# Kernel optimization log

Measured on AMD Instinct MI355X. Metric: run time of the kernel, lower is better.

The kernel has to match this reference:

```python
import jax, jax.numpy as jnp
import numpy as np

N = 100000   # nodes per node type
E = 1000000  # edges per edge type
C = 128      # channels
H = 4        # num_heads
D = C // H   # head_dim


def setup_inputs() -> dict:
    key = jax.random.key(0)
    ks = jax.random.split(key, 16)
    return {
        "x_A": jax.random.normal(ks[0], (N, C), jnp.float32),
        "x_B": jax.random.normal(ks[1], (N, C), jnp.float32),
        "Wq": jax.random.normal(ks[2], (C, C), jnp.float32) * 0.05,
        "bq": jax.random.normal(ks[3], (C,), jnp.float32) * 0.05,
        "Wk": jax.random.normal(ks[4], (C, C), jnp.float32) * 0.05,
        "bk": jax.random.normal(ks[5], (C,), jnp.float32) * 0.05,
        "Wv": jax.random.normal(ks[6], (C, C), jnp.float32) * 0.05,
        "bv": jax.random.normal(ks[7], (C,), jnp.float32) * 0.05,
        "gamma": jnp.ones((C,), jnp.float32),
        "beta": jnp.zeros((C,), jnp.float32),
        "bias_AB": jax.random.normal(ks[8], (1,), jnp.float32),
        "bias_BA": jax.random.normal(ks[9], (1,), jnp.float32),
        "sb_AB": jax.random.normal(ks[10], (E,), jnp.float32),
        "sb_BA": jax.random.normal(ks[11], (E,), jnp.float32),
        "edge_index_AB": jax.random.randint(ks[12], (2, E), 0, N, jnp.int32),
        "edge_index_BA": jax.random.randint(ks[13], (2, E), 0, N, jnp.int32),
    }


def _edge_attention(x_src, x_dst, src, dst, sb, etype_bias, Wq, bq, Wk, bk, Wv, bv):
    """Per-edge-type attention: gather -> score -> dst-segment softmax -> scatter-add."""
    n_dst = x_dst.shape[0]
    Q = (x_dst @ Wq.T + bq).reshape(n_dst, H, D)
    K = (x_src @ Wk.T + bk).reshape(-1, H, D)
    V = (x_src @ Wv.T + bv).reshape(-1, H, D)
    # [E, H] per-edge scores
    scores = jnp.einsum('ehd,ehd->eh', Q[dst], K[src]) / np.float32(np.sqrt(D))
    scores = scores + sb[:, None] + etype_bias  # spatial bias + edge-type bias
    # segment softmax over edges grouped by dst node (numerically stable)
    m = jax.ops.segment_max(scores, dst, num_segments=n_dst)
    ex = jnp.exp(scores - m[dst])
    denom = jax.ops.segment_sum(ex, dst, num_segments=n_dst)
    w = ex / denom[dst]  # [E, H]
    msg = (V[src] * w[:, :, None]).reshape(-1, C)  # [E, C]
    return jax.ops.segment_sum(msg, dst, num_segments=n_dst)  # index_add_


def _layernorm(x, gamma, beta, eps=1e-5):
    mu = x.mean(-1, keepdims=True)
    var = ((x - mu) ** 2).mean(-1, keepdims=True)
    return (x - mu) / jnp.sqrt(var + eps) * gamma + beta


def _forward(x_A, x_B, Wq, bq, Wk, bk, Wv, bv, gamma, beta,
             bias_AB, bias_BA, sb_AB, sb_BA, edge_index_AB, edge_index_BA):
    src_ab, dst_ab = edge_index_AB[0], edge_index_AB[1]  # A -> B
    src_ba, dst_ba = edge_index_BA[0], edge_index_BA[1]  # B -> A
    lin = (Wq, bq, Wk, bk, Wv, bv)
    out_B = _edge_attention(x_A, x_B, src_ab, dst_ab, sb_AB, bias_AB, *lin)
    out_A = _edge_attention(x_B, x_A, src_ba, dst_ba, sb_BA, bias_BA, *lin)
    # total degree = in_deg + out_deg per node type
    ones_e = jnp.ones((E,), jnp.float32)
    deg_A = (jax.ops.segment_sum(ones_e, src_ab, num_segments=N)
             + jax.ops.segment_sum(ones_e, dst_ba, num_segments=N))
    deg_B = (jax.ops.segment_sum(ones_e, dst_ab, num_segments=N)
             + jax.ops.segment_sum(ones_e, src_ba, num_segments=N))
    out_A = out_A + deg_A[:, None]
    out_B = out_B + deg_B[:, None]
    out_A = _layernorm(out_A + x_A, gamma, beta)
    out_B = _layernorm(out_B + x_B, gamma, beta)
    return out_A, out_B


def reference(x_A, x_B, Wq, bq, Wk, bk, Wv, bv, gamma, beta,
              bias_AB, bias_BA, sb_AB, sb_BA, edge_index_AB, edge_index_BA):
    return _forward(x_A, x_B, Wq, bq, Wk, bk, Wv, bv, gamma, beta,
                    bias_AB, bias_BA, sb_AB, sb_BA, edge_index_AB, edge_index_BA)
```

## Files before the change

### kernel.cpp

```cpp
#include <hip/hip_runtime.h>

#define CH 128
#define QSCALE (0.17677669529663687f * 1.4426950408889634f)
#define LOG2E 1.4426950408889634f
#define SCAN_BLK 1024
#define KVSTRIDE 384
#define QROWS 32
#define WCVT_BLOCKS 192

typedef _Float16 f16;
typedef _Float16 f16x2 __attribute__((ext_vector_type(2)));
typedef _Float16 f16x8 __attribute__((ext_vector_type(8)));
typedef __attribute__((ext_vector_type(4))) float f32x4;

__device__ __forceinline__ unsigned pk2(float a, float b) {
    auto h = __builtin_amdgcn_cvt_pkrtz(a, b);
    return __builtin_bit_cast(unsigned, h);
}
__device__ __forceinline__ f16x2 u2h(unsigned u) { return __builtin_bit_cast(f16x2, u); }

template <int CTRL>
__device__ __forceinline__ float dpp_add(float x) {
    const int t = __builtin_amdgcn_update_dpp(0, __builtin_bit_cast(int, x), CTRL, 0xF, 0xF, false);
    return x + __builtin_bit_cast(float, t);
}
__device__ __forceinline__ float head_sum(float x) {
    x = dpp_add<0xB1>(x);
    x = dpp_add<0x4E>(x);
    x = dpp_add<0x124>(x);
    x = dpp_add<0x128>(x);
    return x;
}

__global__ __launch_bounds__(256) void wcvt_hist(
    const float* __restrict__ Wq, const float* __restrict__ Wk, const float* __restrict__ Wv,
    unsigned short* __restrict__ Wb,
    const int* __restrict__ eiAB, const int* __restrict__ eiBA,
    int* __restrict__ degAB, int* __restrict__ degBA,
    int nE, int ebl)
{
    if ((int)blockIdx.x < WCVT_BLOCKS) {
        const int i = blockIdx.x * 256 + threadIdx.x;
        const float* W = (i < CH * CH) ? Wq : (i < 2 * CH * CH) ? Wk : Wv;
        const float s = (i < CH * CH) ? QSCALE : 1.f;
        f16 h = (f16)(W[i & (CH * CH - 1)] * s);
        Wb[i] = __builtin_bit_cast(unsigned short, h);
        return;
    }
    const int b = blockIdx.x - WCVT_BLOCKS;
    const int dir = b >= ebl;
    const int e = ((b - dir * ebl) * 256 + threadIdx.x) * 4;
    if (e >= nE) return;
    const int* ei = dir ? eiBA : eiAB;
    int* deg = dir ? degBA : degAB;
    if (e + 3 < nE) {
        const int4 d4 = *(const int4*)(ei + nE + e);
        atomicAdd(&deg[d4.x], 1); atomicAdd(&deg[d4.y], 1);
        atomicAdd(&deg[d4.z], 1); atomicAdd(&deg[d4.w], 1);
    } else {
        for (int j = e; j < nE; ++j) atomicAdd(&deg[ei[nE + j]], 1);
    }
}

__global__ __launch_bounds__(256) void scan_local(const int* __restrict__ degAB, const int* __restrict__ degBA,
                                                  int* __restrict__ offsAB, int* __restrict__ offsBA,
                                                  int* __restrict__ bsums, int n, int nb)
{
    __shared__ int s[256];
    const int dir = blockIdx.x >= nb;
    const int blk = blockIdx.x - dir * nb;
    const int* deg = dir ? degBA : degAB;
    int* offs = dir ? offsBA : offsAB;
    int* bs = bsums + dir * 256;

    const int t = threadIdx.x;
    const int base = blk * SCAN_BLK + t * 4;
    int v0 = 0, v1 = 0, v2 = 0, v3 = 0;
    if (base + 3 < n) {
        int4 q = *(const int4*)(deg + base);
        v0 = q.x; v1 = q.y; v2 = q.z; v3 = q.w;
    } else {
        if (base + 0 < n) v0 = deg[base + 0];
        if (base + 1 < n) v1 = deg[base + 1];
        if (base + 2 < n) v2 = deg[base + 2];
    }
    const int tsum = v0 + v1 + v2 + v3;
    s[t] = tsum;
    __syncthreads();
    for (int off = 1; off < 256; off <<= 1) {
        int add = (t >= off) ? s[t - off] : 0;
        __syncthreads();
        s[t] += add;
        __syncthreads();
    }
    const int excl = s[t] - tsum;
    if (base + 0 < n) offs[base + 0] = excl;
    if (base + 1 < n) offs[base + 1] = excl + v0;
    if (base + 2 < n) offs[base + 2] = excl + v0 + v1;
    if (base + 3 < n) offs[base + 3] = excl + v0 + v1 + v2;
    if (t == 255) bs[blk] = s[255];
}

__global__ __launch_bounds__(256) void add_bsums(int* __restrict__ offsAB, int* __restrict__ offsBA,
                                                 int* __restrict__ curAB, int* __restrict__ curBA,
                                                 const int* __restrict__ bsums, int n, int nbl, int nb)
{
    __shared__ int s[256];
    const int dir = blockIdx.x >= nbl;
    const int blk = blockIdx.x - dir * nbl;
    const int t = threadIdx.x;
    int v = (t < nb) ? bsums[dir * 256 + t] : 0;
    s[t] = v;
    __syncthreads();
    for (int off = 1; off < 256; off <<= 1) {
        int add = (t >= off) ? s[t - off] : 0;
        __syncthreads();
        s[t] += add;
        __syncthreads();
    }
    const int i = blk * 256 + t;
    if (i >= n) return;
    const int bi = i >> 10;
    const int excl = (bi == 0) ? 0 : s[bi - 1];
    int* offs = dir ? offsBA : offsAB;
    int* cur  = dir ? curBA  : curAB;
    const int vv = offs[i] + excl;
    offs[i] = vv;
    cur[i] = vv;
}

__global__ __launch_bounds__(256) void qkv_csr(
    const float* __restrict__ xA, const float* __restrict__ xB,
    const unsigned short* __restrict__ Wb,
    const float* __restrict__ bq, const float* __restrict__ bk, const float* __restrict__ bv,
    unsigned short* __restrict__ Qb,
    unsigned char* __restrict__ KVb,
    const int* __restrict__ eiAB, const int* __restrict__ eiBA,
    const float* __restrict__ sbAB, const float* __restrict__ sbBA,
    const float* __restrict__ biasAB, const float* __restrict__ biasBA,
    int* __restrict__ curAB, int* __restrict__ curBA,
    int2* __restrict__ edAB, int2* __restrict__ edBA,
    int n, int nE, int cblocks, int ebl)
{
    __shared__ __align__(16) char lds[8192];

    const int bid = blockIdx.x;
    const int mixed = 4 * cblocks;
    int ridx; bool is_csr;
    if (bid < mixed) {
        const int g = bid >> 2, r = bid & 3;
        is_csr = (r == 3);
        ridx = is_csr ? g : g * 3 + r;
    } else {
        is_csr = false;
        ridx = 3 * cblocks + (bid - mixed);
    }

    if (is_csr) {
        const int dir = ridx >= ebl;
        const int e = ((ridx - dir * ebl) * 256 + threadIdx.x) * 4;
        if (e >= nE) return;
        const int* ei = dir ? eiBA : eiAB;
        const float* sb = dir ? sbBA : sbAB;
        const float bia = dir ? biasBA[0] : biasAB[0];
        int* cur = dir ? curBA : curAB;
        int2* ed = dir ? edBA : edAB;
        if (e + 3 < nE) {
            const int4 s4 = *(const int4*)(ei + e);
            const int4 d4 = *(const int4*)(ei + nE + e);
            const float4 b4 = *(const float4*)(sb + e);
            int p0 = atomicAdd(&cur[d4.x], 1); ed[p0] = make_int2(s4.x * KVSTRIDE, __float_as_int((b4.x + bia) * LOG2E));
            int p1 = atomicAdd(&cur[d4.y], 1); ed[p1] = make_int2(s4.y * KVSTRIDE, __float_as_int((b4.y + bia) * LOG2E));
            int p2 = atomicAdd(&cur[d4.z], 1); ed[p2] = make_int2(s4.z * KVSTRIDE, __float_as_int((b4.z + bia) * LOG2E));
            int p3 = atomicAdd(&cur[d4.w], 1); ed[p3] = make_int2(s4.w * KVSTRIDE, __float_as_int((b4.w + bia) * LOG2E));
        } else {
            for (int j = e; j < nE; ++j) {
                const int pos = atomicAdd(&cur[ei[nE + j]], 1);
                ed[pos] = make_int2(ei[j] * KVSTRIDE, __float_as_int((sb[j] + bia) * LOG2E));
            }
        }
        return;
    }

    const int type = ridx & 1;
    const float* x = type ? xB : xA;
    const int bRow = (ridx >> 1) * QROWS;
    const int tid = threadIdx.x;

    #pragma unroll
    for (int j = 0; j < 4; ++j) {
        const int flat16 = j * 256 + tid;
        const int row = flat16 >> 5;
        const int c16 = flat16 & 31;
        float4 v = make_float4(0.f, 0.f, 0.f, 0.f);
        if (bRow + row < n) v = *(const float4*)(x + (size_t)(bRow + row) * CH + c16 * 4);
        const int off = (row * 256 + c16 * 8) ^ ((row & 7) << 4);
        *(uint2*)(lds + off) = make_uint2(pk2(v.x, v.y), pk2(v.z, v.w));
    }
    __syncthreads();

    const int w = tid >> 6, l = tid & 63, lr = l & 15, lg = l >> 4;
    const int colbase = w * 32;

    f32x4 acc[3][2][2];
    #pragma unroll
    for (int p = 0; p < 3; ++p)
        #pragma unroll
        for (int ct = 0; ct < 2; ++ct)
            #pragma unroll
            for (int rt = 0; rt < 2; ++rt)
                acc[p][ct][rt] = (f32x4){0.f, 0.f, 0.f, 0.f};

    #pragma unroll
    for (int kt = 0; kt < 4; ++kt) {
        f16x8 bx[2];
        #pragma unroll
        for (int rt = 0; rt < 2; ++rt) {
            const int row = rt * 16 + lr;
            const int off = (row * 256 + kt * 64 + lg * 16) ^ ((row & 7) << 4);
            bx[rt] = *(const f16x8*)(lds + off);
        }
        #pragma unroll
        for (int p = 0; p < 3; ++p) {
            #pragma unroll
            for (int ct = 0; ct < 2; ++ct) {
                const int ocol = colbase + ct * 16 + lr;
                const f16x8 a = *(const f16x8*)(Wb + ((size_t)p << 14) + (size_t)ocol * CH + kt * 32 + lg * 8);
                #pragma unroll
                for (int rt = 0; rt < 2; ++rt)
                    acc[p][ct][rt] = __builtin_amdgcn_mfma_f32_16x16x32_f16(a, bx[rt], acc[p][ct][rt], 0, 0, 0);
            }
        }
    }

    unsigned short* Qo = Qb + (size_t)type * n * CH;
    unsigned char* KVo = KVb + (size_t)type * n * KVSTRIDE;

    #pragma unroll
    for (int p = 0; p < 3; ++p) {
        __syncthreads();
        const float* bias = (p == 0) ? bq : (p == 1) ? bk : bv;
        #pragma unroll
        for (int ct = 0; ct < 2; ++ct) {
            const int c0 = colbase + ct * 16 + lg * 4;
            float4 bb = *(const float4*)(bias + c0);
            if (p == 0) { bb.x *= QSCALE; bb.y *= QSCALE; bb.z *= QSCALE; bb.w *= QSCALE; }
            #pragma unroll
            for (int rt = 0; rt < 2; ++rt) {
                const int nl = rt * 16 + lr;
                const int swz = (nl & 7) << 4;
                const f32x4 a4 = acc[p][ct][rt];
                if (p == 1) {
                    const int cbk = w * 32 + ct * 16 + lg * 4;
                    int kw = __builtin_amdgcn_cvt_pk_fp8_f32(a4[0] + bb.x, a4[1] + bb.y, 0, false);
                    kw     = __builtin_amdgcn_cvt_pk_fp8_f32(a4[2] + bb.z, a4[3] + bb.w, kw, true);
                    *(unsigned*)(lds + nl * 128 + (cbk ^ swz)) = (unsigned)kw;
                } else {
                    const int cbq = w * 64 + ct * 32 + lg * 8;
                    *(uint2*)(lds + nl * 256 + (cbq ^ swz)) =
                        make_uint2(pk2(a4[0] + bb.x, a4[1] + bb.y), pk2(a4[2] + bb.z, a4[3] + bb.w));
                }
            }
        }
        __syncthreads();
        if (p == 1) {
            const int row = tid >> 3, c = tid & 7;
            const uint4 val = *(const uint4*)(lds + row * 128 + ((c ^ (row & 7)) << 4));
            const int node = bRow + row;
            if (node < n) *(uint4*)(KVo + (size_t)node * KVSTRIDE + c * 16) = val;
        } else {
            #pragma unroll
            for (int j = 0; j < 2; ++j) {
                const int flat = j * 256 + tid;
                const int row = flat >> 4, c16 = flat & 15;
                const uint4 val = *(const uint4*)(lds + row * 256 + ((c16 ^ (row & 7)) << 4));
                const int node = bRow + row;
                if (node < n) {
                    if (p == 0) *(uint4*)(Qo + (size_t)node * CH + c16 * 8) = val;
                    else        *(uint4*)(KVo + (size_t)node * KVSTRIDE + 128 + c16 * 16) = val;
                }
            }
        }
    }
}

__global__ __launch_bounds__(256) void attn_node(
    const unsigned short* __restrict__ Qb,
    const unsigned char* __restrict__ KVb,
    const float* __restrict__ xA, const float* __restrict__ xB,
    const int* __restrict__ offsAB, const int* __restrict__ offsBA,
    const int* __restrict__ degAB, const int* __restrict__ degBA,
    const int2* __restrict__ edAB, const int2* __restrict__ edBA,
    const float* __restrict__ gamma, const float* __restrict__ beta,
    float* __restrict__ out, int n, int abl)
{
    const int dir = blockIdx.x >= abl;
    const int node = (blockIdx.x - dir * abl) * 4 + (threadIdx.x >> 6);
    if (node >= n) return;
    const int l = threadIdx.x & 63;
    const int l2 = l * 2;

    const unsigned short* Q = Qb + (size_t)dir * n * CH;
    const unsigned char* KV = KVb + (size_t)(1 - dir) * n * KVSTRIDE;
    const float* x = dir ? xB : xA;
    const int* offs = dir ? offsAB : offsBA;
    const int* deg  = dir ? degAB  : degBA;
    const int2* ed  = dir ? edAB   : edBA;
    float* o = out + (size_t)dir * n * CH;

    const f16x2 qp = u2h(*(const unsigned*)(Q + (size_t)node * CH + l2));
    const float qf0 = (float)qp[0], qf1 = (float)qp[1];

    const int beg = __builtin_amdgcn_readfirstlane(offs[node]);
    const int d   = __builtin_amdgcn_readfirstlane(deg[node]);

    float m = -3.0e38f, den = 0.f;
    f16x2 a01 = (f16x2){(f16)0.f, (f16)0.f};

    auto loadE = [&](int i, float& sbf, unsigned& kc, unsigned& vc) {
        if (i < d) {
            const int2 e = ed[beg + i];
            sbf = __int_as_float(e.y);
            const unsigned b = (unsigned)e.x;
            kc = *(const unsigned short*)(KV + b + l2);
            vc = *(const unsigned*)(KV + b + 128 + l2 * 2);
        } else {
            sbf = __int_as_float((int)0xFF800000u);
            kc = 0; vc = 0;
        }
    };

    auto procPair = [&](float sf0, unsigned k0, unsigned v0,
                        float sf1, unsigned k1, unsigned v1) {
        const auto kf0 = __builtin_amdgcn_cvt_pk_f32_fp8((int)k0, false);
        const auto kf1 = __builtin_amdgcn_cvt_pk_f32_fp8((int)k1, false);
        float sa = head_sum(fmaf(qf0, kf0[0], qf1 * kf0[1])) + sf0;
        float sb = head_sum(fmaf(qf0, kf1[0], qf1 * kf1[1])) + sf1;
        const float pm = fmaxf(sa, sb);
        if (!__all(pm <= m + 8.f)) {
            const float mn = fmaxf(m, pm);
            const float sc = exp2f(m - mn);
            den *= sc;
            a01 *= u2h(pk2(sc, sc));
            m = mn;
        }
        const float ea = exp2f(sa - m);
        const float eb = exp2f(sb - m);
        den += ea + eb;
        a01 += u2h(pk2(ea, ea)) * u2h(v0);
        a01 += u2h(pk2(eb, eb)) * u2h(v1);
    };

    float sA0, sA1, sA2, sA3, sB0, sB1, sB2, sB3;
    unsigned kA0, kA1, kA2, kA3, kB0, kB1, kB2, kB3;
    unsigned vA0, vA1, vA2, vA3, vB0, vB1, vB2, vB3;
    loadE(0, sA0, kA0, vA0); loadE(1, sA1, kA1, vA1);
    loadE(2, sA2, kA2, vA2); loadE(3, sA3, kA3, vA3);
    loadE(4, sB0, kB0, vB0); loadE(5, sB1, kB1, vB1);
    loadE(6, sB2, kB2, vB2); loadE(7, sB3, kB3, vB3);

    for (int i = 0; i < d; i += 8) {
        procPair(sA0, kA0, vA0, sA1, kA1, vA1);
        procPair(sA2, kA2, vA2, sA3, kA3, vA3);
        loadE(i + 8,  sA0, kA0, vA0); loadE(i + 9,  sA1, kA1, vA1);
        loadE(i + 10, sA2, kA2, vA2); loadE(i + 11, sA3, kA3, vA3);
        if (i + 4 >= d) break;
        procPair(sB0, kB0, vB0, sB1, kB1, vB1);
        procPair(sB2, kB2, vB2, sB3, kB3, vB3);
        loadE(i + 12, sB0, kB0, vB0); loadE(i + 13, sB1, kB1, vB1);
        loadE(i + 14, sB2, kB2, vB2); loadE(i + 15, sB3, kB3, vB3);
    }

    const float inv = (den > 0.f) ? 1.f / den : 0.f;
    const float2 xv = *(const float2*)(x + (size_t)node * CH + l2);
    const float w0 = (float)a01[0] * inv + xv.x;
    const float w1 = (float)a01[1] * inv + xv.y;

    float sum = w0 + w1;
    #pragma unroll
    for (int off = 32; off; off >>= 1) sum += __shfl_xor(sum, off);
    const float mean = sum * (1.f / 128.f);
    const float c0 = w0 - mean, c1 = w1 - mean;
    float vs = c0 * c0 + c1 * c1;
    #pragma unroll
    for (int off = 32; off; off >>= 1) vs += __shfl_xor(vs, off);
    const float rstd = rsqrtf(vs * (1.f / 128.f) + 1e-5f);

    const float2 g = *(const float2*)(gamma + l2);
    const float2 bt = *(const float2*)(beta + l2);
    float2 ov;
    ov.x = c0 * rstd * g.x + bt.x;
    ov.y = c1 * rstd * g.y + bt.y;
    *(float2*)(o + (size_t)node * CH + l2) = ov;
}

extern "C" void kernel_launch(void* const* d_in, const int* in_sizes, int n_in,
                              void* d_out, int out_size, void* d_ws, size_t ws_size,
                              hipStream_t stream)
{
    const float* xA     = (const float*)d_in[0];
    const float* xB     = (const float*)d_in[1];
    const float* Wq     = (const float*)d_in[2];
    const float* bq     = (const float*)d_in[3];
    const float* Wk     = (const float*)d_in[4];
    const float* bk     = (const float*)d_in[5];
    const float* Wv     = (const float*)d_in[6];
    const float* bv     = (const float*)d_in[7];
    const float* gamma  = (const float*)d_in[8];
    const float* beta   = (const float*)d_in[9];
    const float* biasAB = (const float*)d_in[10];
    const float* biasBA = (const float*)d_in[11];
    const float* sbAB   = (const float*)d_in[12];
    const float* sbBA   = (const float*)d_in[13];
    const int*   eiAB   = (const int*)d_in[14];
    const int*   eiBA   = (const int*)d_in[15];

    const int n  = in_sizes[0] / CH;
    const int nE = in_sizes[12];
    const size_t NC = (size_t)n * CH;

    char* p = (char*)d_ws;
    auto carve = [&](size_t bytes) { char* r = p; p += (bytes + 15) & ~(size_t)15; return r; };
    unsigned short* Qb = (unsigned short*)carve(2 * NC * 2);
    unsigned char*  KVb = (unsigned char*)carve((size_t)2 * n * KVSTRIDE);
    unsigned short* Wb  = (unsigned short*)carve(3 * CH * CH * 2);
    int2* edAB  = (int2*)carve((size_t)nE * 8);
    int2* edBA  = (int2*)carve((size_t)nE * 8);
    int* offsAB = (int*)carve((size_t)n * 4);
    int* offsBA = (int*)carve((size_t)n * 4);
    int* degAB  = (int*)carve((size_t)2 * n * 4);
    int* degBA  = degAB + n;
    int* curAB  = (int*)carve((size_t)n * 4);
    int* curBA  = (int*)carve((size_t)n * 4);
    int* bsums  = (int*)carve(2 * 256 * 4);

    float* out = (float*)d_out;

    (void)hipMemsetAsync(degAB, 0, (size_t)2 * n * sizeof(int), stream);

    const int ebl4 = (nE + 1023) / 1024;
    wcvt_hist<<<WCVT_BLOCKS + 2 * ebl4, 256, 0, stream>>>(Wq, Wk, Wv, Wb,
                                                          eiAB, eiBA, degAB, degBA, nE, ebl4);

    const int nb = (n + SCAN_BLK - 1) / SCAN_BLK;
    scan_local<<<2 * nb, 256, 0, stream>>>(degAB, degBA, offsAB, offsBA, bsums, n, nb);
    const int nbl = (n + 255) / 256;
    add_bsums<<<2 * nbl, 256, 0, stream>>>(offsAB, offsBA, curAB, curBA, bsums, n, nbl, nb);

    const int qblocks = 2 * ((n + QROWS - 1) / QROWS);
    const int cblocks = 2 * ebl4;
    qkv_csr<<<qblocks + cblocks, 256, 0, stream>>>(xA, xB, Wb, bq, bk, bv, Qb, KVb,
                                                   eiAB, eiBA, sbAB, sbBA, biasAB, biasBA,
                                                   curAB, curBA, edAB, edBA,
                                                   n, nE, cblocks, ebl4);

    const int abl = (n + 3) / 4;
    attn_node<<<2 * abl, 256, 0, stream>>>(Qb, KVb, xA, xB, offsAB, offsBA, degAB, degBA,
                                           edAB, edBA, gamma, beta, out, n, abl);
}
```

Measured before the change: 418.4 us.

## Split CSR fill across kernels to overlap with QKV and first attention pass

The CSR fill for the BA edges now runs alongside the QKV projection. The fill for the AB edges is moved into a combined kernel that also runs attention for node type A, with CSR blocks interleaved among attention blocks. Attention for node type B then runs in a separate final kernel that depends on the AB CSR. The aim is to hide the atomic scatter cost behind compute and spread the load better, at the price of one extra launch and changed block-interleave ratios.

```diff
diff --git a/kernel.cpp b/kernel.cpp
--- a/kernel.cpp
+++ b/kernel.cpp
@@ -30,6 +30,126 @@
     x = dpp_add<0x124>(x);
     x = dpp_add<0x128>(x);
     return x;
+}
+
+
+__device__ __forceinline__ void csr_body(int ridx, const int* __restrict__ ei,
+                                         const float* __restrict__ sb, float bia,
+                                         int* __restrict__ cur, int2* __restrict__ ed, int nE)
+{
+    const int e = (ridx * 256 + threadIdx.x) * 4;
+    if (e >= nE) return;
+    if (e + 3 < nE) {
+        const int4 s4 = *(const int4*)(ei + e);
+        const int4 d4 = *(const int4*)(ei + nE + e);
+        const float4 b4 = *(const float4*)(sb + e);
+        int p0 = atomicAdd(&cur[d4.x], 1); ed[p0] = make_int2(s4.x * KVSTRIDE, __float_as_int((b4.x + bia) * LOG2E));
+        int p1 = atomicAdd(&cur[d4.y], 1); ed[p1] = make_int2(s4.y * KVSTRIDE, __float_as_int((b4.y + bia) * LOG2E));
+        int p2 = atomicAdd(&cur[d4.z], 1); ed[p2] = make_int2(s4.z * KVSTRIDE, __float_as_int((b4.z + bia) * LOG2E));
+        int p3 = atomicAdd(&cur[d4.w], 1); ed[p3] = make_int2(s4.w * KVSTRIDE, __float_as_int((b4.w + bia) * LOG2E));
+    } else {
+        for (int j = e; j < nE; ++j) {
+            const int pos = atomicAdd(&cur[ei[nE + j]], 1);
+            ed[pos] = make_int2(ei[j] * KVSTRIDE, __float_as_int((sb[j] + bia) * LOG2E));
+        }
+    }
+}
+
+__device__ __forceinline__ void attn_body(int nblk,
+    const unsigned short* __restrict__ Q, const unsigned char* __restrict__ KV,
+    const float* __restrict__ x, const int* __restrict__ offs, const int* __restrict__ deg,
+    const int2* __restrict__ ed, const float* __restrict__ gamma, const float* __restrict__ beta,
+    float* __restrict__ o, int n)
+{
+    const int node = nblk * 4 + (threadIdx.x >> 6);
+    if (node >= n) return;
+    const int l = threadIdx.x & 63;
+    const int l2 = l * 2;
+
+    const f16x2 qp = u2h(*(const unsigned*)(Q + (size_t)node * CH + l2));
+    const float qf0 = (float)qp[0], qf1 = (float)qp[1];
+
+    const int beg = __builtin_amdgcn_readfirstlane(offs[node]);
+    const int d   = __builtin_amdgcn_readfirstlane(deg[node]);
+
+    float m = -3.0e38f, den = 0.f;
+    f16x2 a01 = (f16x2){(f16)0.f, (f16)0.f};
+
+    auto loadE = [&](int i, float& sbf, unsigned& kc, unsigned& vc) {
+        if (i < d) {
+            const int2 e = ed[beg + i];
+            sbf = __int_as_float(e.y);
+            const unsigned b = (unsigned)e.x;
+            kc = *(const unsigned short*)(KV + b + l2);
+            vc = *(const unsigned*)(KV + b + 128 + l2 * 2);
+        } else {
+            sbf = __int_as_float((int)0xFF800000u);
+            kc = 0; vc = 0;
+        }
+    };
+
+    auto procPair = [&](float sf0, unsigned k0, unsigned v0,
+                        float sf1, unsigned k1, unsigned v1) {
+        const auto kf0 = __builtin_amdgcn_cvt_pk_f32_fp8((int)k0, false);
+        const auto kf1 = __builtin_amdgcn_cvt_pk_f32_fp8((int)k1, false);
+        float sa = head_sum(fmaf(qf0, kf0[0], qf1 * kf0[1])) + sf0;
+        float sb = head_sum(fmaf(qf0, kf1[0], qf1 * kf1[1])) + sf1;
+        const float pm = fmaxf(sa, sb);
+        if (!__all(pm <= m + 8.f)) {
+            const float mn = fmaxf(m, pm);
+            const float sc = exp2f(m - mn);
+            den *= sc;
+            a01 *= u2h(pk2(sc, sc));
+            m = mn;
+        }
+        const float ea = exp2f(sa - m);
+        const float eb = exp2f(sb - m);
+        den += ea + eb;
+        a01 += u2h(pk2(ea, ea)) * u2h(v0);
+        a01 += u2h(pk2(eb, eb)) * u2h(v1);
+    };
+
+    float sA0, sA1, sA2, sA3, sB0, sB1, sB2, sB3;
+    unsigned kA0, kA1, kA2, kA3, kB0, kB1, kB2, kB3;
+    unsigned vA0, vA1, vA2, vA3, vB0, vB1, vB2, vB3;
+    loadE(0, sA0, kA0, vA0); loadE(1, sA1, kA1, vA1);
+    loadE(2, sA2, kA2, vA2); loadE(3, sA3, kA3, vA3);
+    loadE(4, sB0, kB0, vB0); loadE(5, sB1, kB1, vB1);
+    loadE(6, sB2, kB2, vB2); loadE(7, sB3, kB3, vB3);
+
+    for (int i = 0; i < d; i += 8) {
+        procPair(sA0, kA0, vA0, sA1, kA1, vA1);
+        procPair(sA2, kA2, vA2, sA3, kA3, vA3);
+        loadE(i + 8,  sA0, kA0, vA0); loadE(i + 9,  sA1, kA1, vA1);
+        loadE(i + 10, sA2, kA2, vA2); loadE(i + 11, sA3, kA3, vA3);
+        if (i + 4 >= d) break;
+        procPair(sB0, kB0, vB0, sB1, kB1, vB1);
+        procPair(sB2, kB2, vB2, sB3, kB3, vB3);
+        loadE(i + 12, sB0, kB0, vB0); loadE(i + 13, sB1, kB1, vB1);
+        loadE(i + 14, sB2, kB2, vB2); loadE(i + 15, sB3, kB3, vB3);
+    }
+
+    const float inv = (den > 0.f) ? 1.f / den : 0.f;
+    const float2 xv = *(const float2*)(x + (size_t)node * CH + l2);
+    const float w0 = (float)a01[0] * inv + xv.x;
+    const float w1 = (float)a01[1] * inv + xv.y;
+
+    float sum = w0 + w1;
+    #pragma unroll
+    for (int off = 32; off; off >>= 1) sum += __shfl_xor(sum, off);
+    const float mean = sum * (1.f / 128.f);
+    const float c0 = w0 - mean, c1 = w1 - mean;
+    float vs = c0 * c0 + c1 * c1;
+    #pragma unroll
+    for (int off = 32; off; off >>= 1) vs += __shfl_xor(vs, off);
+    const float rstd = rsqrtf(vs * (1.f / 128.f) + 1e-5f);
+
+    const float2 g = *(const float2*)(gamma + l2);
+    const float2 bt = *(const float2*)(beta + l2);
+    float2 ov;
+    ov.x = c0 * rstd * g.x + bt.x;
+    ov.y = c1 * rstd * g.y + bt.y;
+    *(float2*)(o + (size_t)node * CH + l2) = ov;
 }
 
 __global__ __launch_bounds__(256) void wcvt_hist(
@@ -129,56 +249,31 @@
     cur[i] = vv;
 }
 
-__global__ __launch_bounds__(256) void qkv_csr(
+__global__ __launch_bounds__(256) void qkv_csr1(
     const float* __restrict__ xA, const float* __restrict__ xB,
     const unsigned short* __restrict__ Wb,
     const float* __restrict__ bq, const float* __restrict__ bk, const float* __restrict__ bv,
-    unsigned short* __restrict__ Qb,
-    unsigned char* __restrict__ KVb,
-    const int* __restrict__ eiAB, const int* __restrict__ eiBA,
-    const float* __restrict__ sbAB, const float* __restrict__ sbBA,
-    const float* __restrict__ biasAB, const float* __restrict__ biasBA,
-    int* __restrict__ curAB, int* __restrict__ curBA,
-    int2* __restrict__ edAB, int2* __restrict__ edBA,
-    int n, int nE, int cblocks, int ebl)
+    unsigned short* __restrict__ Qb, unsigned char* __restrict__ KVb,
+    const int* __restrict__ eiBA, const float* __restrict__ sbBA, const float* __restrict__ biasBA,
+    int* __restrict__ curBA, int2* __restrict__ edBA,
+    int n, int nE, int cblocks, int qblocks)
 {
     __shared__ __align__(16) char lds[8192];
 
     const int bid = blockIdx.x;
-    const int mixed = 4 * cblocks;
+    const int mixed = 7 * cblocks;
     int ridx; bool is_csr;
     if (bid < mixed) {
-        const int g = bid >> 2, r = bid & 3;
-        is_csr = (r == 3);
-        ridx = is_csr ? g : g * 3 + r;
+        const int g = bid / 7, r = bid % 7;
+        is_csr = (r == 6);
+        ridx = is_csr ? g : g * 6 + r;
     } else {
         is_csr = false;
-        ridx = 3 * cblocks + (bid - mixed);
+        ridx = 6 * cblocks + (bid - mixed);
     }
 
     if (is_csr) {
-        const int dir = ridx >= ebl;
-        const int e = ((ridx - dir * ebl) * 256 + threadIdx.x) * 4;
-        if (e >= nE) return;
-        const int* ei = dir ? eiBA : eiAB;
-        const float* sb = dir ? sbBA : sbAB;
-        const float bia = dir ? biasBA[0] : biasAB[0];
-        int* cur = dir ? curBA : curAB;
-        int2* ed = dir ? edBA : edAB;
-        if (e + 3 < nE) {
-            const int4 s4 = *(const int4*)(ei + e);
-            const int4 d4 = *(const int4*)(ei + nE + e);
-            const float4 b4 = *(const float4*)(sb + e);
-            int p0 = atomicAdd(&cur[d4.x], 1); ed[p0] = make_int2(s4.x * KVSTRIDE, __float_as_int((b4.x + bia) * LOG2E));
-            int p1 = atomicAdd(&cur[d4.y], 1); ed[p1] = make_int2(s4.y * KVSTRIDE, __float_as_int((b4.y + bia) * LOG2E));
-            int p2 = atomicAdd(&cur[d4.z], 1); ed[p2] = make_int2(s4.z * KVSTRIDE, __float_as_int((b4.z + bia) * LOG2E));
-            int p3 = atomicAdd(&cur[d4.w], 1); ed[p3] = make_int2(s4.w * KVSTRIDE, __float_as_int((b4.w + bia) * LOG2E));
-        } else {
-            for (int j = e; j < nE; ++j) {
-                const int pos = atomicAdd(&cur[ei[nE + j]], 1);
-                ed[pos] = make_int2(ei[j] * KVSTRIDE, __float_as_int((sb[j] + bia) * LOG2E));
-            }
-        }
+        csr_body(ridx, eiBA, sbBA, biasBA[0], curBA, edBA, nE);
         return;
     }
 
@@ -284,114 +379,43 @@
     }
 }
 
-__global__ __launch_bounds__(256) void attn_node(
-    const unsigned short* __restrict__ Qb,
-    const unsigned char* __restrict__ KVb,
-    const float* __restrict__ xA, const float* __restrict__ xB,
-    const int* __restrict__ offsAB, const int* __restrict__ offsBA,
-    const int* __restrict__ degAB, const int* __restrict__ degBA,
-    const int2* __restrict__ edAB, const int2* __restrict__ edBA,
-    const float* __restrict__ gamma, const float* __restrict__ beta,
-    float* __restrict__ out, int n, int abl)
-{
-    const int dir = blockIdx.x >= abl;
-    const int node = (blockIdx.x - dir * abl) * 4 + (threadIdx.x >> 6);
-    if (node >= n) return;
-    const int l = threadIdx.x & 63;
-    const int l2 = l * 2;
-
-    const unsigned short* Q = Qb + (size_t)dir * n * CH;
-    const unsigned char* KV = KVb + (size_t)(1 - dir) * n * KVSTRIDE;
-    const float* x = dir ? xB : xA;
-    const int* offs = dir ? offsAB : offsBA;
-    const int* deg  = dir ? degAB  : degBA;
-    const int2* ed  = dir ? edAB   : edBA;
-    float* o = out + (size_t)dir * n * CH;
-
-    const f16x2 qp = u2h(*(const unsigned*)(Q + (size_t)node * CH + l2));
-    const float qf0 = (float)qp[0], qf1 = (float)qp[1];
-
-    const int beg = __builtin_amdgcn_readfirstlane(offs[node]);
-    const int d   = __builtin_amdgcn_readfirstlane(deg[node]);
-
-    float m = -3.0e38f, den = 0.f;
-    f16x2 a01 = (f16x2){(f16)0.f, (f16)0.f};
-
-    auto loadE = [&](int i, float& sbf, unsigned& kc, unsigned& vc) {
-        if (i < d) {
-            const int2 e = ed[beg + i];
-            sbf = __int_as_float(e.y);
-            const unsigned b = (unsigned)e.x;
-            kc = *(const unsigned short*)(KV + b + l2);
-            vc = *(const unsigned*)(KV + b + 128 + l2 * 2);
-        } else {
-            sbf = __int_as_float((int)0xFF800000u);
-            kc = 0; vc = 0;
-        }
-    };
-
-    auto procPair = [&](float sf0, unsigned k0, unsigned v0,
-                        float sf1, unsigned k1, unsigned v1) {
-        const auto kf0 = __builtin_amdgcn_cvt_pk_f32_fp8((int)k0, false);
-        const auto kf1 = __builtin_amdgcn_cvt_pk_f32_fp8((int)k1, false);
-        float sa = head_sum(fmaf(qf0, kf0[0], qf1 * kf0[1])) + sf0;
-        float sb = head_sum(fmaf(qf0, kf1[0], qf1 * kf1[1])) + sf1;
-        const float pm = fmaxf(sa, sb);
-        if (!__all(pm <= m + 8.f)) {
-            const float mn = fmaxf(m, pm);
-            const float sc = exp2f(m - mn);
-            den *= sc;
-            a01 *= u2h(pk2(sc, sc));
-            m = mn;
-        }
-        const float ea = exp2f(sa - m);
-        const float eb = exp2f(sb - m);
-        den += ea + eb;
-        a01 += u2h(pk2(ea, ea)) * u2h(v0);
-        a01 += u2h(pk2(eb, eb)) * u2h(v1);
-    };
-
-    float sA0, sA1, sA2, sA3, sB0, sB1, sB2, sB3;
-    unsigned kA0, kA1, kA2, kA3, kB0, kB1, kB2, kB3;
-    unsigned vA0, vA1, vA2, vA3, vB0, vB1, vB2, vB3;
-    loadE(0, sA0, kA0, vA0); loadE(1, sA1, kA1, vA1);
-    loadE(2, sA2, kA2, vA2); loadE(3, sA3, kA3, vA3);
-    loadE(4, sB0, kB0, vB0); loadE(5, sB1, kB1, vB1);
-    loadE(6, sB2, kB2, vB2); loadE(7, sB3, kB3, vB3);
-
-    for (int i = 0; i < d; i += 8) {
-        procPair(sA0, kA0, vA0, sA1, kA1, vA1);
-        procPair(sA2, kA2, vA2, sA3, kA3, vA3);
-        loadE(i + 8,  sA0, kA0, vA0); loadE(i + 9,  sA1, kA1, vA1);
-        loadE(i + 10, sA2, kA2, vA2); loadE(i + 11, sA3, kA3, vA3);
-        if (i + 4 >= d) break;
-        procPair(sB0, kB0, vB0, sB1, kB1, vB1);
-        procPair(sB2, kB2, vB2, sB3, kB3, vB3);
-        loadE(i + 12, sB0, kB0, vB0); loadE(i + 13, sB1, kB1, vB1);
-        loadE(i + 14, sB2, kB2, vB2); loadE(i + 15, sB3, kB3, vB3);
-    }
-
-    const float inv = (den > 0.f) ? 1.f / den : 0.f;
-    const float2 xv = *(const float2*)(x + (size_t)node * CH + l2);
-    const float w0 = (float)a01[0] * inv + xv.x;
-    const float w1 = (float)a01[1] * inv + xv.y;
-
-    float sum = w0 + w1;
-    #pragma unroll
-    for (int off = 32; off; off >>= 1) sum += __shfl_xor(sum, off);
-    const float mean = sum * (1.f / 128.f);
-    const float c0 = w0 - mean, c1 = w1 - mean;
-    float vs = c0 * c0 + c1 * c1;
-    #pragma unroll
-    for (int off = 32; off; off >>= 1) vs += __shfl_xor(vs, off);
-    const float rstd = rsqrtf(vs * (1.f / 128.f) + 1e-5f);
-
-    const float2 g = *(const float2*)(gamma + l2);
-    const float2 bt = *(const float2*)(beta + l2);
-    float2 ov;
-    ov.x = c0 * rstd * g.x + bt.x;
-    ov.y = c1 * rstd * g.y + bt.y;
-    *(float2*)(o + (size_t)node * CH + l2) = ov;
+__global__ __launch_bounds__(256) void attn_csr2(
+    const unsigned short* __restrict__ Qb, const unsigned char* __restrict__ KVb,
+    const float* __restrict__ xA,
+    const int* __restrict__ offsBA, const int* __restrict__ degBA, const int2* __restrict__ edBA,
+    const float* __restrict__ gamma, const float* __restrict__ beta, float* __restrict__ out,
+    const int* __restrict__ eiAB, const float* __restrict__ sbAB, const float* __restrict__ biasAB,
+    int* __restrict__ curAB, int2* __restrict__ edAB,
+    int n, int nE, int cblocks)
+{
+    const int bid = blockIdx.x;
+    const int mixed = 26 * cblocks;
+    int ridx; bool is_csr;
+    if (bid < mixed) {
+        const int g = bid / 26, r = bid % 26;
+        is_csr = (r == 25);
+        ridx = is_csr ? g : g * 25 + r;
+    } else {
+        is_csr = false;
+        ridx = 25 * cblocks + (bid - mixed);
+    }
+
+    if (is_csr) {
+        csr_body(ridx, eiAB, sbAB, biasAB[0], curAB, edAB, nE);
+        return;
+    }
+    attn_body(ridx, Qb, KVb + (size_t)n * KVSTRIDE, xA, offsBA, degBA, edBA, gamma, beta, out, n);
+}
+
+__global__ __launch_bounds__(256) void attn_one(
+    const unsigned short* __restrict__ Qb, const unsigned char* __restrict__ KVb,
+    const float* __restrict__ xB,
+    const int* __restrict__ offsAB, const int* __restrict__ degAB, const int2* __restrict__ edAB,
+    const float* __restrict__ gamma, const float* __restrict__ beta, float* __restrict__ out,
+    int n)
+{
+    attn_body(blockIdx.x, Qb + (size_t)n * CH, KVb, xB, offsAB, degAB, edAB,
+              gamma, beta, out + (size_t)n * CH, n);
 }
 
 extern "C" void kernel_launch(void* const* d_in, const int* in_sizes, int n_in,
@@ -448,13 +472,15 @@
     add_bsums<<<2 * nbl, 256, 0, stream>>>(offsAB, offsBA, curAB, curBA, bsums, n, nbl, nb);
 
     const int qblocks = 2 * ((n + QROWS - 1) / QROWS);
-    const int cblocks = 2 * ebl4;
-    qkv_csr<<<qblocks + cblocks, 256, 0, stream>>>(xA, xB, Wb, bq, bk, bv, Qb, KVb,
-                                                   eiAB, eiBA, sbAB, sbBA, biasAB, biasBA,
-                                                   curAB, curBA, edAB, edBA,
-                                                   n, nE, cblocks, ebl4);
+    qkv_csr1<<<qblocks + ebl4, 256, 0, stream>>>(xA, xB, Wb, bq, bk, bv, Qb, KVb,
+                                                 eiBA, sbBA, biasBA, curBA, edBA,
+                                                 n, nE, ebl4, qblocks);
 
     const int abl = (n + 3) / 4;
-    attn_node<<<2 * abl, 256, 0, stream>>>(Qb, KVb, xA, xB, offsAB, offsBA, degAB, degBA,
-                                           edAB, edBA, gamma, beta, out, n, abl);
-}
+    attn_csr2<<<abl + ebl4, 256, 0, stream>>>(Qb, KVb, xA, offsBA, degBA, edBA,
+                                              gamma, beta, out,
+                                              eiAB, sbAB, biasAB, curAB, edAB,
+                                              n, nE, ebl4);
+
+    attn_one<<<abl, 256, 0, stream>>>(Qb, KVb, xB, offsAB, degAB, edAB, gamma, beta, out, n);
+}
```

Measured after the change: 433.7 us. 1.04x slower.
